# Optimization experiments

Hardware: AMD Instinct MI355X
Metric: run time of the kernel (lower is better)

The kernel has to match this reference:

```python
import jax, jax.numpy as jnp
import numpy as np

SCALING = 16.0 / 8.0  # alpha / rank
GAMMA = 1.0
EPS = 1e-12


def setup_inputs() -> dict:
    key = jax.random.key(0)
    ks = jax.random.split(key, 8)
    B, T, H, O = 4, 2048, 4096, 4096
    E_tot, E_act, r = 16, 4, 8
    return {
        "x": jax.random.normal(ks[0], (B, T, H), jnp.float32),
        "W_base": jax.random.normal(ks[1], (O, H), jnp.float32) * 0.02,
        "b_base": jax.random.normal(ks[2], (O,), jnp.float32) * 0.02,
        "lora_A": jax.random.normal(ks[3], (E_tot, r, H), jnp.float32) * 0.02,
        "lora_B": jax.random.normal(ks[4], (E_tot, O, r), jnp.float32) * 0.02,
        "router_W": jax.random.normal(ks[5], (E_tot, H), jnp.float32) * 0.02,
        "router_b": jax.random.normal(ks[6], (E_tot,), jnp.float32) * 0.02,
        "domain_prior": jax.random.uniform(ks[7], (E_tot,), jnp.float32),
        "active": jnp.arange(E_act, dtype=jnp.int32),
    }


def reference(x, W_base, b_base, lora_A, lora_B, router_W, router_b, domain_prior, active):
    # Base linear: [B,T,H] @ [H,O] -> [B,T,O]
    y = jnp.einsum('bth,oh->bto', x, W_base) + b_base
    # Gather active experts' low-rank factors
    A = lora_A[active]   # [E, r, H]
    Bm = lora_B[active]  # [E, O, r]
    # Grouped low-rank GEMMs (dropout is identity at inference)
    z = jnp.einsum('bth,erh->bter', x, A)            # [B,T,E,r]
    contribs = jnp.einsum('bter,eor->bteo', z, Bm) * SCALING  # [B,T,E,O]
    # Token router logits over all experts, restricted to active set
    logits = jnp.einsum('bth,eh->bte', x, router_W) + router_b  # [B,T,E_tot]
    logits = logits[..., active]                                 # [B,T,E]
    prior = domain_prior[active]                                 # [E]
    alpha = jax.nn.softmax(jnp.log(prior + EPS) + logits / GAMMA, axis=-1)  # [B,T,E]
    return y + jnp.einsum('bteo,bte->bto', contribs, alpha)
```

## Files before the change

kernel.cpp:

```cpp
#include <hip/hip_runtime.h>
#include <hip/hip_bf16.h>


typedef _Float16 f16x8 __attribute__((ext_vector_type(8)));
typedef float    f32x4 __attribute__((ext_vector_type(4)));

constexpr int H  = 4096;
constexpr int O  = 4096;
constexpr int KP = 4160;
constexpr int EA = 4;
constexpr float SCALING_F = 2.0f;

typedef const __attribute__((address_space(1))) void gvoid;
typedef __attribute__((address_space(3))) void svoid;

__device__ inline void gload16(const void* g, void* s) {
  __builtin_amdgcn_global_load_lds((gvoid*)g, (svoid*)s, 16, 0, 0);
}

__global__ __launch_bounds__(256) void convert_w3_kernel(
    const float* __restrict__ W, const float* __restrict__ lora_B,
    const float* __restrict__ lora_A, const float* __restrict__ router_W,
    const int* __restrict__ active, _Float16* __restrict__ wh,
    _Float16* __restrict__ vh) {
  const int bid = blockIdx.x;
  const int tid = threadIdx.x;
  if (bid < O) {
    const int o = bid;
    const float* wrow = W + (size_t)o * H;
    _Float16* dstrow = wh + (size_t)o * KP;
    for (int g = tid; g < 520; g += 256) {
      const int k = g * 8;
      float v[8];
      if (k < H) {
        float4 a = *(const float4*)(wrow + k), b = *(const float4*)(wrow + k + 4);
        v[0] = a.x; v[1] = a.y; v[2] = a.z; v[3] = a.w;
        v[4] = b.x; v[5] = b.y; v[6] = b.z; v[7] = b.w;
      } else if (k < H + 32) {
        const int e = (k - H) >> 3;
        const float* s = lora_B + ((size_t)active[e] * O + o) * 8;
        float4 a = *(const float4*)s, b = *(const float4*)(s + 4);
        v[0] = a.x; v[1] = a.y; v[2] = a.z; v[3] = a.w;
        v[4] = b.x; v[5] = b.y; v[6] = b.z; v[7] = b.w;
      } else {
#pragma unroll
        for (int i = 0; i < 8; ++i) v[i] = 0.f;
      }
      f16x8 h;
#pragma unroll
      for (int i = 0; i < 8; ++i) h[i] = (_Float16)v[i];
      *(f16x8*)(dstrow + k) = h;
    }
  } else {
    const int j = bid - O;
    const float* src = nullptr;
    if (j < 32)      src = lora_A + (size_t)(active[j >> 3] * 8 + (j & 7)) * H;
    else if (j < 36) src = router_W + (size_t)active[j - 32] * H;
    _Float16* dstrow = vh + (size_t)j * H;
    for (int g = tid; g < 512; g += 256) {
      const int k = g * 8;
      f16x8 h;
      if (src) {
        float4 a = *(const float4*)(src + k), b = *(const float4*)(src + k + 4);
        h[0] = (_Float16)a.x; h[1] = (_Float16)a.y;
        h[2] = (_Float16)a.z; h[3] = (_Float16)a.w;
        h[4] = (_Float16)b.x; h[5] = (_Float16)b.y;
        h[6] = (_Float16)b.z; h[7] = (_Float16)b.w;
      } else {
#pragma unroll
        for (int i = 0; i < 8; ++i) h[i] = (_Float16)0.f;
      }
      *(f16x8*)(dstrow + k) = h;
    }
  }
}

__global__ __launch_bounds__(256) void router_fused4_kernel(
    const float* __restrict__ x, const _Float16* __restrict__ vh,
    const float* __restrict__ router_b, const float* __restrict__ prior,
    const int* __restrict__ active, _Float16* __restrict__ xh) {
  __shared__ float zred[4][16][48];
  const int tid  = threadIdx.x;
  const int lane = tid & 63;
  const int w    = tid >> 6;
  const long t0  = (long)blockIdx.x * 16;
  const int r15  = lane & 15;
  const int kg   = lane >> 4;

  const float*    xp  = x  + (t0 + r15) * H  + w * 32 + kg * 8;
  _Float16*       xhp = xh + (t0 + r15) * KP + w * 32 + kg * 8;
  const _Float16* vp  = vh + (size_t)r15 * H + w * 32 + kg * 8;

  f32x4 acc[3];
  const f32x4 zero = {0.f, 0.f, 0.f, 0.f};
  acc[0] = zero; acc[1] = zero; acc[2] = zero;

#pragma unroll 2
  for (int c = 0; c < 32; ++c) {
    const int ko = c * 128;
    float4 v0 = *(const float4*)(xp + ko);
    float4 v1 = *(const float4*)(xp + ko + 4);
    f16x8 a;
    a[0] = (_Float16)v0.x; a[1] = (_Float16)v0.y;
    a[2] = (_Float16)v0.z; a[3] = (_Float16)v0.w;
    a[4] = (_Float16)v1.x; a[5] = (_Float16)v1.y;
    a[6] = (_Float16)v1.z; a[7] = (_Float16)v1.w;
    *(f16x8*)(xhp + ko) = a;
#pragma unroll
    for (int nf = 0; nf < 3; ++nf) {
      f16x8 b = *(const f16x8*)(vp + (size_t)nf * 16 * H + ko);
      acc[nf] = __builtin_amdgcn_mfma_f32_16x16x32_f16(a, b, acc[nf], 0, 0, 0);
    }
  }

#pragma unroll
  for (int nf = 0; nf < 3; ++nf)
#pragma unroll
    for (int r = 0; r < 4; ++r)
      zred[w][kg * 4 + r][nf * 16 + r15] = acc[nf][r];
  __syncthreads();

  float s[3];
#pragma unroll
  for (int j = 0; j < 3; ++j) {
    const int sl = tid + 256 * j;
    const int tt = sl / 48, jj = sl % 48;
    s[j] = zred[0][tt][jj] + zred[1][tt][jj] + zred[2][tt][jj] + zred[3][tt][jj];
  }
  __syncthreads();
#pragma unroll
  for (int j = 0; j < 3; ++j) {
    const int sl = tid + 256 * j;
    zred[0][sl / 48][sl % 48] = s[j];
  }
  __syncthreads();

  if (tid < 16 * EA) {
    const int tt = tid >> 2, e = tid & 3;
    const float* zt = &zred[0][tt][0];
    float le[EA], mx = -1e30f;
#pragma unroll
    for (int e2 = 0; e2 < EA; ++e2) {
      const int ae = active[e2];
      le[e2] = logf(prior[ae] + 1e-12f) + zt[32 + e2] + router_b[ae];
      mx = fmaxf(mx, le[e2]);
    }
    float sum = 0.f;
#pragma unroll
    for (int e2 = 0; e2 < EA; ++e2) sum += expf(le[e2] - mx);
    const float a = expf(le[e] - mx) / sum * SCALING_F;
    f16x8 ch, zz;
#pragma unroll
    for (int r = 0; r < 8; ++r) {
      ch[r] = (_Float16)(a * zt[e * 8 + r]);
      zz[r] = (_Float16)0.f;
    }
    _Float16* xr = xh + (t0 + tt) * KP + H;
    *(f16x8*)(xr + e * 8) = ch;
    *(f16x8*)(xr + 32 + e * 8) = zz;
  }
}

constexpr int BM = 128, BN = 128, BK = 64, NT = KP / BK;

__global__ __launch_bounds__(256) void gemm_kernel(
    const _Float16* __restrict__ xh, const _Float16* __restrict__ wh,
    const float* __restrict__ b_base, float* __restrict__ out) {
  __shared__ _Float16 As[2][BM * BK];
  __shared__ _Float16 Ws[2][BN * BK];
  const int tid  = threadIdx.x;
  const int lane = tid & 63;
  const int wave = tid >> 6;
  const int bid  = (int)blockIdx.x;
  const int im = bid >> 5;
  const int in = bid & 31;
  const size_t trow0 = (size_t)im * BM;
  const size_t ocol0 = (size_t)in * BN;
  const int wr = wave >> 1, wc = wave & 1;

  f32x4 acc[4][4];
  const f32x4 zero = {0.f, 0.f, 0.f, 0.f};
#pragma unroll
  for (int m = 0; m < 4; ++m)
#pragma unroll
    for (int n = 0; n < 4; ++n) acc[m][n] = zero;

  const int srow  = lane >> 3;
  const int sslot = (lane & 7) ^ srow;
  const int r15 = lane & 15;
  const int kg  = lane >> 4;

  auto stage = [&](int b, int t) {
    const int k0 = t * BK;
#pragma unroll
    for (int i = 0; i < 8; ++i) {
      const int ch  = wave + 4 * i;
      const int sub = ch & 15;
      const int row = sub * 8 + srow;
      if (ch < 16)
        gload16(xh + (trow0 + row) * KP + k0 + sslot * 8, &As[b][sub * 512]);
      else
        gload16(wh + (ocol0 + row) * KP + k0 + sslot * 8, &Ws[b][sub * 512]);
    }
  };

  stage(0, 0);
  for (int t = 0; t < NT; ++t) {
    const int b = t & 1;
    if (t + 1 < NT) {
      stage(b ^ 1, t + 1);
      asm volatile("s_waitcnt vmcnt(8)" ::: "memory");
    } else {
      asm volatile("s_waitcnt vmcnt(0)" ::: "memory");
    }
    __builtin_amdgcn_s_barrier();
#pragma unroll
    for (int kk = 0; kk < 2; ++kk) {
      f16x8 a[4], bfr[4];
#pragma unroll
      for (int m = 0; m < 4; ++m) {
        const int row  = wr * 64 + m * 16 + r15;
        const int slot = (kk * 4 + kg) ^ (row & 7);
        a[m] = *(const f16x8*)(&As[b][row * 64 + slot * 8]);
      }
#pragma unroll
      for (int n = 0; n < 4; ++n) {
        const int row  = wc * 64 + n * 16 + r15;
        const int slot = (kk * 4 + kg) ^ (row & 7);
        bfr[n] = *(const f16x8*)(&Ws[b][row * 64 + slot * 8]);
      }
#pragma unroll
      for (int m = 0; m < 4; ++m)
#pragma unroll
        for (int n = 0; n < 4; ++n)
          acc[m][n] = __builtin_amdgcn_mfma_f32_16x16x32_f16(a[m], bfr[n], acc[m][n], 0, 0, 0);
    }
    __builtin_amdgcn_s_barrier();
  }

#pragma unroll
  for (int n = 0; n < 4; ++n) {
    const size_t col = ocol0 + wc * 64 + n * 16 + r15;
    const float bb = b_base[col];
#pragma unroll
    for (int m = 0; m < 4; ++m) {
      const size_t row = trow0 + wr * 64 + m * 16 + kg * 4;
#pragma unroll
      for (int j = 0; j < 4; ++j)
        out[(row + j) * O + col] = acc[m][n][j] + bb;
    }
  }
}

extern "C" void kernel_launch(void* const* d_in, const int* in_sizes, int n_in,
                              void* d_out, int out_size, void* d_ws, size_t ws_size,
                              hipStream_t stream) {
  const float* x        = (const float*)d_in[0];
  const float* W_base   = (const float*)d_in[1];
  const float* b_base   = (const float*)d_in[2];
  const float* lora_A   = (const float*)d_in[3];
  const float* lora_B   = (const float*)d_in[4];
  const float* router_W = (const float*)d_in[5];
  const float* router_b = (const float*)d_in[6];
  const float* prior    = (const float*)d_in[7];
  const int*   active   = (const int*)d_in[8];
  float* out = (float*)d_out;

  const int M = in_sizes[0] / H;

  char* ws = (char*)d_ws;
  _Float16* xh = (_Float16*)ws;
  _Float16* wh = (_Float16*)(ws + (size_t)M * KP * 2);
  _Float16* vh = (_Float16*)(ws + (size_t)M * KP * 2 + (size_t)O * KP * 2);

  convert_w3_kernel<<<O + 48, 256, 0, stream>>>(W_base, lora_B, lora_A, router_W,
                                                active, wh, vh);
  router_fused4_kernel<<<M / 16, 256, 0, stream>>>(x, vh, router_b, prior, active, xh);
  gemm_kernel<<<(M / BM) * (O / BN), 256, 0, stream>>>(xh, wh, b_base, out);
}
```

Baseline: 612.5 us.

## Widen router kernel to 16 waves and single-buffer the GEMM LDS staging

The router/convert kernel now runs 1024 threads per block, so 16 waves split the K dimension with 256 elements each instead of 4 waves striding over all of K, and the cross-wave reduction grows to 16 partial sums. Separately, the main GEMM drops its double-buffered LDS pipeline with manual vmcnt waits and uses a single buffer with __syncthreads before and after each load. The wider router block is meant to cut per-thread serial work and latency. The single buffer halves LDS use, which may allow more resident blocks, but it exposes global-load latency because loads no longer overlap the MFMA work.

```diff
diff --git a/kernel.cpp b/kernel.cpp
--- a/kernel.cpp
+++ b/kernel.cpp
@@ -75,11 +75,13 @@
   }
 }
 
-__global__ __launch_bounds__(256) void router_fused4_kernel(
+constexpr int RW5 = 16;
+
+__global__ __launch_bounds__(1024) void router_fused5_kernel(
     const float* __restrict__ x, const _Float16* __restrict__ vh,
     const float* __restrict__ router_b, const float* __restrict__ prior,
     const int* __restrict__ active, _Float16* __restrict__ xh) {
-  __shared__ float zred[4][16][48];
+  __shared__ float zred[RW5][16][48];
   const int tid  = threadIdx.x;
   const int lane = tid & 63;
   const int w    = tid >> 6;
@@ -87,17 +89,17 @@
   const int r15  = lane & 15;
   const int kg   = lane >> 4;
 
-  const float*    xp  = x  + (t0 + r15) * H  + w * 32 + kg * 8;
-  _Float16*       xhp = xh + (t0 + r15) * KP + w * 32 + kg * 8;
-  const _Float16* vp  = vh + (size_t)r15 * H + w * 32 + kg * 8;
+  const float*    xp  = x  + (t0 + r15) * H  + w * 256 + kg * 8;
+  _Float16*       xhp = xh + (t0 + r15) * KP + w * 256 + kg * 8;
+  const _Float16* vp  = vh + (size_t)r15 * H + w * 256 + kg * 8;
 
   f32x4 acc[3];
   const f32x4 zero = {0.f, 0.f, 0.f, 0.f};
   acc[0] = zero; acc[1] = zero; acc[2] = zero;
 
-#pragma unroll 2
-  for (int c = 0; c < 32; ++c) {
-    const int ko = c * 128;
+#pragma unroll
+  for (int c = 0; c < 8; ++c) {
+    const int ko = c * 32;
     float4 v0 = *(const float4*)(xp + ko);
     float4 v1 = *(const float4*)(xp + ko + 4);
     f16x8 a;
@@ -120,24 +122,20 @@
       zred[w][kg * 4 + r][nf * 16 + r15] = acc[nf][r];
   __syncthreads();
 
-  float s[3];
-#pragma unroll
-  for (int j = 0; j < 3; ++j) {
-    const int sl = tid + 256 * j;
-    const int tt = sl / 48, jj = sl % 48;
-    s[j] = zred[0][tt][jj] + zred[1][tt][jj] + zred[2][tt][jj] + zred[3][tt][jj];
+  float s = 0.f;
+  int tt = 0, jj = 0;
+  if (tid < 16 * 48) {
+    tt = tid / 48; jj = tid % 48;
+#pragma unroll
+    for (int ww = 0; ww < RW5; ++ww) s += zred[ww][tt][jj];
   }
   __syncthreads();
-#pragma unroll
-  for (int j = 0; j < 3; ++j) {
-    const int sl = tid + 256 * j;
-    zred[0][sl / 48][sl % 48] = s[j];
-  }
+  if (tid < 16 * 48) zred[0][tt][jj] = s;
   __syncthreads();
 
   if (tid < 16 * EA) {
-    const int tt = tid >> 2, e = tid & 3;
-    const float* zt = &zred[0][tt][0];
+    const int t2 = tid >> 2, e = tid & 3;
+    const float* zt = &zred[0][t2][0];
     float le[EA], mx = -1e30f;
 #pragma unroll
     for (int e2 = 0; e2 < EA; ++e2) {
@@ -155,25 +153,24 @@
       ch[r] = (_Float16)(a * zt[e * 8 + r]);
       zz[r] = (_Float16)0.f;
     }
-    _Float16* xr = xh + (t0 + tt) * KP + H;
+    _Float16* xr = xh + (t0 + t2) * KP + H;
     *(f16x8*)(xr + e * 8) = ch;
     *(f16x8*)(xr + 32 + e * 8) = zz;
   }
 }
 
-constexpr int BM = 128, BN = 128, BK = 64, NT = KP / BK;
+constexpr int BM = 128, BN = 128, BK = 64;
 
 __global__ __launch_bounds__(256) void gemm_kernel(
     const _Float16* __restrict__ xh, const _Float16* __restrict__ wh,
     const float* __restrict__ b_base, float* __restrict__ out) {
-  __shared__ _Float16 As[2][BM * BK];
-  __shared__ _Float16 Ws[2][BN * BK];
+  __shared__ _Float16 As[BM * BK];
+  __shared__ _Float16 Ws[BN * BK];
   const int tid  = threadIdx.x;
   const int lane = tid & 63;
   const int wave = tid >> 6;
-  const int bid  = (int)blockIdx.x;
-  const int im = bid >> 5;
-  const int in = bid & 31;
+  const int im = (int)(blockIdx.x >> 5);
+  const int in = (int)(blockIdx.x & 31);
   const size_t trow0 = (size_t)im * BM;
   const size_t ocol0 = (size_t)in * BN;
   const int wr = wave >> 1, wc = wave & 1;
@@ -190,54 +187,42 @@
   const int r15 = lane & 15;
   const int kg  = lane >> 4;
 
-  auto stage = [&](int b, int t) {
-    const int k0 = t * BK;
+  for (int step = 0; step < KP / BK; ++step) {
+    const int k0 = step * BK;
+    __syncthreads();
 #pragma unroll
     for (int i = 0; i < 8; ++i) {
       const int ch  = wave + 4 * i;
       const int sub = ch & 15;
       const int row = sub * 8 + srow;
       if (ch < 16)
-        gload16(xh + (trow0 + row) * KP + k0 + sslot * 8, &As[b][sub * 512]);
+        gload16(xh + (trow0 + row) * KP + k0 + sslot * 8, As + sub * 512);
       else
-        gload16(wh + (ocol0 + row) * KP + k0 + sslot * 8, &Ws[b][sub * 512]);
-    }
-  };
-
-  stage(0, 0);
-  for (int t = 0; t < NT; ++t) {
-    const int b = t & 1;
-    if (t + 1 < NT) {
-      stage(b ^ 1, t + 1);
-      asm volatile("s_waitcnt vmcnt(8)" ::: "memory");
-    } else {
-      asm volatile("s_waitcnt vmcnt(0)" ::: "memory");
-    }
-    __builtin_amdgcn_s_barrier();
+        gload16(wh + (ocol0 + row) * KP + k0 + sslot * 8, Ws + sub * 512);
+    }
+    __syncthreads();
 #pragma unroll
     for (int kk = 0; kk < 2; ++kk) {
-      f16x8 a[4], bfr[4];
+      f16x8 a[4], b[4];
 #pragma unroll
       for (int m = 0; m < 4; ++m) {
         const int row  = wr * 64 + m * 16 + r15;
         const int slot = (kk * 4 + kg) ^ (row & 7);
-        a[m] = *(const f16x8*)(&As[b][row * 64 + slot * 8]);
+        a[m] = *(const f16x8*)(As + row * 64 + slot * 8);
       }
 #pragma unroll
       for (int n = 0; n < 4; ++n) {
         const int row  = wc * 64 + n * 16 + r15;
         const int slot = (kk * 4 + kg) ^ (row & 7);
-        bfr[n] = *(const f16x8*)(&Ws[b][row * 64 + slot * 8]);
+        b[n] = *(const f16x8*)(Ws + row * 64 + slot * 8);
       }
 #pragma unroll
       for (int m = 0; m < 4; ++m)
 #pragma unroll
         for (int n = 0; n < 4; ++n)
-          acc[m][n] = __builtin_amdgcn_mfma_f32_16x16x32_f16(a[m], bfr[n], acc[m][n], 0, 0, 0);
-    }
-    __builtin_amdgcn_s_barrier();
-  }
-
+          acc[m][n] = __builtin_amdgcn_mfma_f32_16x16x32_f16(a[m], b[n], acc[m][n], 0, 0, 0);
+    }
+  }
 #pragma unroll
   for (int n = 0; n < 4; ++n) {
     const size_t col = ocol0 + wc * 64 + n * 16 + r15;
@@ -275,6 +260,6 @@
 
   convert_w3_kernel<<<O + 48, 256, 0, stream>>>(W_base, lora_B, lora_A, router_W,
                                                 active, wh, vh);
-  router_fused4_kernel<<<M / 16, 256, 0, stream>>>(x, vh, router_b, prior, active, xh);
+  router_fused5_kernel<<<M / 16, 1024, 0, stream>>>(x, vh, router_b, prior, active, xh);
   gemm_kernel<<<(M / BM) * (O / BN), 256, 0, stream>>>(xh, wh, b_base, out);
 }
```

New measurement: 593.0 us. 1.03x faster.
